# Kernel tuning notes

Hardware: AMD Instinct MI355X
Metric: run time of the kernel (lower is better)

Reference implementation:

```python
import jax, jax.numpy as jnp
import numpy as np

HIDDEN = 768
NUM_HEADS = 12
HEAD_DIM = HIDDEN // NUM_HEADS
B, S = 4, 2048


def setup_inputs() -> dict:
    key = jax.random.key(0)
    ks = jax.random.split(key, 10)
    scale = 1.0 / np.sqrt(HIDDEN)
    return {
        "hidden_states": jax.random.normal(ks[0], (B, S, HIDDEN), dtype=jnp.float32),
        "attention_mask": jnp.ones((B, S), dtype=jnp.float32),
        "Wq": jax.random.normal(ks[1], (HIDDEN, HIDDEN), dtype=jnp.float32) * scale,
        "bq": jnp.zeros((HIDDEN,), dtype=jnp.float32),
        "Wk": jax.random.normal(ks[2], (HIDDEN, HIDDEN), dtype=jnp.float32) * scale,
        "bk": jnp.zeros((HIDDEN,), dtype=jnp.float32),
        "Wv": jax.random.normal(ks[3], (HIDDEN, HIDDEN), dtype=jnp.float32) * scale,
        "bv": jnp.zeros((HIDDEN,), dtype=jnp.float32),
        "Wo": jax.random.normal(ks[4], (HIDDEN, HIDDEN), dtype=jnp.float32) * scale,
        "bo": jnp.zeros((HIDDEN,), dtype=jnp.float32),
    }


def reference(hidden_states, attention_mask, Wq, bq, Wk, bk, Wv, bv, Wo, bo):
    b, s, _ = hidden_states.shape
    # nn.Linear: x @ W.T + b  (W is [out, in])
    Q = hidden_states @ Wq.T + bq
    K = hidden_states @ Wk.T + bk
    V = hidden_states @ Wv.T + bv
    # [b, s, h*d] -> [b, h, s, d]
    Q = Q.reshape(b, s, NUM_HEADS, HEAD_DIM).transpose(0, 2, 1, 3)
    K = K.reshape(b, s, NUM_HEADS, HEAD_DIM).transpose(0, 2, 1, 3)
    V = V.reshape(b, s, NUM_HEADS, HEAD_DIM).transpose(0, 2, 1, 3)
    # scores: [b, h, s, s]
    scores = jnp.einsum("bhqd,bhkd->bhqk", Q, K) / jnp.sqrt(
        jnp.asarray(HEAD_DIM, dtype=Q.dtype))
    # mask: [b, s] -> additive bias broadcast over heads and query dim
    bias = (1.0 - attention_mask)[:, None, None, :] * -10000.0
    scores = scores + bias
    probs = jax.nn.softmax(scores, axis=-1)  # dropout p=0.0 -> identity
    context = jnp.einsum("bhqk,bhkd->bhqd", probs, V)
    context = context.transpose(0, 2, 1, 3).reshape(b, s, HIDDEN)
    return context @ Wo.T + bo
```

## Files before the change

### kernel.cpp

```cpp
#include <hip/hip_runtime.h>
#include <hip/hip_bf16.h>

#define SEQ   2048
#define NH    12
#define MTOK  8192

typedef __attribute__((ext_vector_type(8))) short short8;
typedef __attribute__((ext_vector_type(4))) short short4v;
typedef __attribute__((ext_vector_type(4))) float f32x4;
typedef __attribute__((ext_vector_type(16))) float f32x16;
typedef __attribute__((ext_vector_type(2))) unsigned uint2v;

__device__ inline short f2bf(float x) {
  __hip_bfloat16 h = __float2bfloat16(x);
  return *(short*)&h;
}

#define GLL(gp, lp) __builtin_amdgcn_global_load_lds( \
    (const __attribute__((address_space(1))) void*)(gp), \
    (__attribute__((address_space(3))) void*)(lp), 16, 0, 0)

#define MFMA(a, b, c) __builtin_amdgcn_mfma_f32_16x16x32_bf16(a, b, c, 0, 0, 0)

#if !defined(__HIP_DEVICE_COMPILE__)
#define MFMA32(a, b, c) (c)
#else
#define MFMA32(a, b, c) __builtin_amdgcn_mfma_f32_32x32x16_bf16(a, b, c, 0, 0, 0)
#endif

#if !defined(__HIP_DEVICE_COMPILE__)
#define EXP2(x) (x)
#elif __has_builtin(__builtin_amdgcn_exp2f)
#define EXP2(x) __builtin_amdgcn_exp2f(x)
#else
#define EXP2(x) __expf((x) * 0.6931471805599453f)
#endif

__device__ inline unsigned pack2bf(float a, float b) {
  unsigned ua = __float_as_uint(a) + 0x8000u;
  unsigned ub = __float_as_uint(b) + 0x8000u;
#if defined(__HIP_DEVICE_COMPILE__) && __has_builtin(__builtin_amdgcn_perm)
  return __builtin_amdgcn_perm(ub, ua, 0x07060302u);
#else
  return (ub & 0xFFFF0000u) | (ua >> 16);
#endif
}

__device__ inline unsigned packtrunc2(float a, float b) {
#if defined(__HIP_DEVICE_COMPILE__) && __has_builtin(__builtin_amdgcn_perm)
  return __builtin_amdgcn_perm(__float_as_uint(b), __float_as_uint(a),
                               0x07060302u);
#else
  return (__float_as_uint(b) & 0xFFFF0000u) | (__float_as_uint(a) >> 16);
#endif
}

__device__ inline uint2v lane32swap(unsigned a, unsigned b) {
#if defined(__HIP_DEVICE_COMPILE__) && __has_builtin(__builtin_amdgcn_permlane32_swap)
  return __builtin_amdgcn_permlane32_swap(a, b, false, false);
#else
  int lane = (int)(threadIdx.x & 63);
  unsigned xa = (unsigned)__shfl((int)a, lane ^ 32, 64);
  unsigned xb = (unsigned)__shfl((int)b, lane ^ 32, 64);
  bool hi = lane >= 32;
  uint2v r;
  r.x = hi ? xb : a;
  r.y = hi ? b : xa;
  return r;
#endif
}

union PackFrag {
  unsigned u[2];
  short4v s;
};

union Frag8 {
  unsigned u[4];
  short8 s;
};

#define QSCALE 0.18033688011112042f
#define MBSCALE -14426.950408889634f

__global__ __launch_bounds__(256) void prep(
    const float* __restrict__ hs, const float* __restrict__ Wq,
    const float* __restrict__ Wk, const float* __restrict__ Wv,
    const float* __restrict__ Wo, const float* __restrict__ mask,
    short* __restrict__ Xb, short* __restrict__ Wqkvb,
    short* __restrict__ Wob, float* __restrict__ mbias) {
  int bid = blockIdx.x;
  if (bid < 6144) {
    int i = bid * 256 + threadIdx.x;
    float4 v = ((const float4*)hs)[i];
    short4v o;
    o[0] = f2bf(v.x); o[1] = f2bf(v.y); o[2] = f2bf(v.z); o[3] = f2bf(v.w);
    ((short4v*)Xb)[i] = o;
  } else if (bid < 6144 + 2304) {
    int idx = (bid - 6144) * 256 + threadIdx.x;
    int r = idx / 192, c = (idx - r * 192) * 4;
    const float* src;
    short* dst;
    int rr;
    if (r < 768)       { src = Wq; rr = r;        dst = Wqkvb; }
    else if (r < 1536) { src = Wk; rr = r - 768;  dst = Wqkvb; }
    else if (r < 2304) { src = Wv; rr = r - 1536; dst = Wqkvb; }
    else               { src = Wo; rr = r - 2304; dst = Wob; r = rr; }
    float4 v = *(const float4*)&src[(size_t)rr * 768 + c];
    short4v o;
    o[0] = f2bf(v.x); o[1] = f2bf(v.y); o[2] = f2bf(v.z); o[3] = f2bf(v.w);
    *(short4v*)&dst[(size_t)r * 768 + c] = o;
  } else {
    int i = (bid - 6144 - 2304) * 256 + threadIdx.x;
    if (i < MTOK) mbias[i] = (1.f - mask[i]) * MBSCALE;
  }
}

#define GEMM_BK64_LOOP(Aptr, Bptr)                                            \
  __shared__ __align__(16) short As[128 * 64];                                \
  __shared__ __align__(16) short Bs[128 * 64];                                \
  const int t = threadIdx.x;                                                  \
  const int wid = t >> 6, lane = t & 63, l15 = lane & 15, quad = lane >> 4;   \
  const int bm = blockIdx.x * 128, bn = blockIdx.y * 128;                     \
  const int mq = (wid & 1) * 64, nq = (wid >> 1) * 64;                        \
  const int srow8 = lane >> 3;                                                \
  const int schunk = lane & 7;                                                \
  const int scol = (schunk ^ srow8) * 8;                                      \
  f32x4 acc[4][4] = {};                                                       \
  const short *gA[4], *gB[4];                                                 \
  _Pragma("unroll") for (int g = 0; g < 4; ++g) {                             \
    int row = wid * 32 + g * 8 + srow8;                                       \
    gA[g] = (Aptr) + (size_t)(bm + row) * 768 + scol;                         \
    gB[g] = (Bptr) + (size_t)(bn + row) * 768 + scol;                         \
  }                                                                           \
  for (int k0 = 0; k0 < 768; k0 += 64) {                                      \
    _Pragma("unroll") for (int g = 0; g < 4; ++g)                             \
      GLL(gA[g] + k0, &As[(wid * 32 + g * 8) * 64]);                          \
    _Pragma("unroll") for (int g = 0; g < 4; ++g)                             \
      GLL(gB[g] + k0, &Bs[(wid * 32 + g * 8) * 64]);                          \
    __syncthreads();                                                          \
    _Pragma("unroll") for (int ks = 0; ks < 2; ++ks) {                        \
      short8 a[4], b[4];                                                      \
      _Pragma("unroll") for (int mt = 0; mt < 4; ++mt)                        \
        a[mt] = *(const short8*)&As[(mq + mt * 16 + l15) * 64 +               \
                                    (((ks * 4 + quad) ^ (l15 & 7)) * 8)];     \
      _Pragma("unroll") for (int nt = 0; nt < 4; ++nt)                        \
        b[nt] = *(const short8*)&Bs[(nq + nt * 16 + l15) * 64 +               \
                                    (((ks * 4 + quad) ^ (l15 & 7)) * 8)];     \
      _Pragma("unroll") for (int mt = 0; mt < 4; ++mt)                        \
        _Pragma("unroll") for (int nt = 0; nt < 4; ++nt)                      \
          acc[mt][nt] = MFMA(a[mt], b[nt], acc[mt][nt]);                      \
    }                                                                         \
    __syncthreads();                                                          \
  }

__global__ __launch_bounds__(256) void gemm_qkv(
    const short* __restrict__ A, const short* __restrict__ B,
    const float* __restrict__ bq, const float* __restrict__ bk,
    const float* __restrict__ bv, short* __restrict__ Qb,
    short* __restrict__ Kb, short* __restrict__ Vt) {
  GEMM_BK64_LOOP(A, B)

  const int seg = bn >= 1536 ? 2 : (bn >= 768 ? 1 : 0);
  const float* bias = seg == 0 ? bq : (seg == 1 ? bk : bv);
  const int colbase = bn - seg * 768;

  if (seg < 2) {
    short* dst = seg == 0 ? Qb : Kb;
    const float sc = seg == 0 ? QSCALE : 1.f;
#pragma unroll
    for (int mt = 0; mt < 4; ++mt)
#pragma unroll
      for (int nt = 0; nt < 4; ++nt) {
        int col = colbase + nq + nt * 16 + l15;
        float bias_v = bias[col];
#pragma unroll
        for (int i = 0; i < 4; ++i) {
          int row = bm + mq + mt * 16 + quad * 4 + i;
          dst[(size_t)row * 768 + col] = f2bf((acc[mt][nt][i] + bias_v) * sc);
        }
      }
  } else {
#pragma unroll
    for (int mt = 0; mt < 4; ++mt) {
      int row0 = bm + mq + mt * 16 + quad * 4;
      int b_ = row0 >> 11, s = row0 & 2047;
#pragma unroll
      for (int nt = 0; nt < 4; ++nt) {
        int col = colbase + nq + nt * 16 + l15;
        float bias_v = bias[col];
        int h = col >> 6, d = col & 63;
        short4v pv;
#pragma unroll
        for (int i = 0; i < 4; ++i) pv[i] = f2bf(acc[mt][nt][i] + bias_v);
        *(short4v*)&Vt[(((size_t)b_ * NH + h) * 64 + d) * 2048 + s] = pv;
      }
    }
  }
}

__global__ __launch_bounds__(256) void gemm_out(
    const short* __restrict__ A, const short* __restrict__ B,
    const float* __restrict__ bias, float* __restrict__ C) {
  GEMM_BK64_LOOP(A, B)

#pragma unroll
  for (int mt = 0; mt < 4; ++mt)
#pragma unroll
    for (int nt = 0; nt < 4; ++nt) {
      int col = bn + nq + nt * 16 + l15;
      float bias_v = bias[col];
#pragma unroll
      for (int i = 0; i < 4; ++i) {
        int row = bm + mq + mt * 16 + quad * 4 + i;
        C[(size_t)row * 768 + col] = acc[mt][nt][i] + bias_v;
      }
    }
}

__global__ __launch_bounds__(256, 3) void attn_v12(
    const short* __restrict__ Qb, const short* __restrict__ Kb,
    const short* __restrict__ Vt, const float* __restrict__ maskb,
    short* __restrict__ Ctx) {
  __shared__ __align__(16) short Ks[2][64 * 64];
  __shared__ __align__(16) short Vs[2][64 * 64];
  const int t = threadIdx.x;
  const int w = t >> 6, lane = t & 63, l31 = lane & 31, hi = lane >> 5;
  const int bh = blockIdx.x, b = bh / NH, h = bh % NH;
  const int q0 = blockIdx.y * 128;

  short8 qb[4];
  {
    int rowq = b * 2048 + q0 + w * 32 + l31;
    const short* qp = &Qb[(size_t)rowq * 768 + h * 64 + hi * 8];
#pragma unroll
    for (int kc = 0; kc < 4; ++kc) qb[kc] = *(const short8*)&qp[kc * 16];
  }

  f32x16 O0 = {}, O1 = {}, lacc = {};
  short8 ones8;
#pragma unroll
  for (int j = 0; j < 8; ++j) ones8[j] = (short)0x3F80;

  const int r0 = w * 16 + (lane >> 3);
  const int pc = lane & 7;
  const int swz0 = (pc ^ (r0 & 7)) * 8;
  const int swz1 = (pc ^ ((r0 + 8) & 7)) * 8;
  const short* gK0 = Kb + (size_t)(b * 2048 + r0) * 768 + h * 64 + swz0;
  const short* gK1 = Kb + (size_t)(b * 2048 + r0 + 8) * 768 + h * 64 + swz1;
  const short* gV0 = Vt + ((size_t)bh * 64 + r0) * 2048 + swz0;
  const short* gV1 = Vt + ((size_t)bh * 64 + r0 + 8) * 2048 + swz1;
  const float* mb = maskb + b * 2048;
  const int rs = l31 & 7;

  GLL(gK0, &Ks[0][(w * 16) * 64]);
  GLL(gK1, &Ks[0][(w * 16 + 8) * 64]);
  GLL(gV0, &Vs[0][(w * 16) * 64]);
  GLL(gV1, &Vs[0][(w * 16 + 8) * 64]);

  for (int ti = 0; ti < 32; ++ti) {
    const int cur = ti & 1;
    const int k0 = ti * 64;
    __syncthreads();

    {
      const size_t kn = (size_t)(((ti + 1) & 31) * 64);
      GLL(gK0 + kn * 768, &Ks[1 - cur][(w * 16) * 64]);
      GLL(gK1 + kn * 768, &Ks[1 - cur][(w * 16 + 8) * 64]);
      GLL(gV0 + kn, &Vs[1 - cur][(w * 16) * 64]);
      GLL(gV1 + kn, &Vs[1 - cur][(w * 16 + 8) * 64]);
    }

    short8 pfrag[4];

#pragma unroll
    for (int kb2 = 0; kb2 < 2; ++kb2) {
      f32x16 S;
#pragma unroll
      for (int g = 0; g < 4; ++g) {
        float4 m4 = *(const float4*)&mb[k0 + kb2 * 32 + g * 8 + hi * 4];
        S[4 * g + 0] = m4.x; S[4 * g + 1] = m4.y;
        S[4 * g + 2] = m4.z; S[4 * g + 3] = m4.w;
      }
#pragma unroll
      for (int kc = 0; kc < 4; ++kc) {
        short8 ka = *(const short8*)&Ks[cur][(kb2 * 32 + l31) * 64 +
                                            (((kc * 2 + hi) ^ rs) * 8)];
        S = MFMA32(ka, qb[kc], S);
      }
      unsigned pk[4][2];
#pragma unroll
      for (int g = 0; g < 4; ++g) {
        float p0 = EXP2(S[4 * g + 0]);
        float p1 = EXP2(S[4 * g + 1]);
        float p2 = EXP2(S[4 * g + 2]);
        float p3 = EXP2(S[4 * g + 3]);
        pk[g][0] = packtrunc2(p0, p1);
        pk[g][1] = packtrunc2(p2, p3);
      }
#pragma unroll
      for (int half = 0; half < 2; ++half) {
        Frag8 f;
        uint2v ra = lane32swap(pk[half * 2][0], pk[half * 2 + 1][0]);
        uint2v rb = lane32swap(pk[half * 2][1], pk[half * 2 + 1][1]);
        f.u[0] = ra.x;
        f.u[1] = rb.x;
        f.u[2] = ra.y;
        f.u[3] = rb.y;
        pfrag[kb2 * 2 + half] = f.s;
      }
    }

#pragma unroll
    for (int c = 0; c < 4; ++c) lacc = MFMA32(ones8, pfrag[c], lacc);

#pragma unroll
    for (int c = 0; c < 4; ++c) {
      short8 av0 = *(const short8*)&Vs[cur][(l31) * 64 +
                                           (((c * 2 + hi) ^ rs) * 8)];
      short8 av1 = *(const short8*)&Vs[cur][(32 + l31) * 64 +
                                           (((c * 2 + hi) ^ rs) * 8)];
      O0 = MFMA32(av0, pfrag[c], O0);
      O1 = MFMA32(av1, pfrag[c], O1);
    }
  }

  {
    float inv = 1.f / lacc[0];
    int rowq = b * 2048 + q0 + w * 32 + l31;
    short* cp = &Ctx[(size_t)rowq * 768 + h * 64 + hi * 4];
#pragma unroll
    for (int g = 0; g < 4; ++g) {
      PackFrag pf0, pf1;
      pf0.u[0] = pack2bf(O0[4 * g + 0] * inv, O0[4 * g + 1] * inv);
      pf0.u[1] = pack2bf(O0[4 * g + 2] * inv, O0[4 * g + 3] * inv);
      *(short4v*)&cp[g * 8] = pf0.s;
      pf1.u[0] = pack2bf(O1[4 * g + 0] * inv, O1[4 * g + 1] * inv);
      pf1.u[1] = pack2bf(O1[4 * g + 2] * inv, O1[4 * g + 3] * inv);
      *(short4v*)&cp[32 + g * 8] = pf1.s;
    }
  }
}

extern "C" void kernel_launch(void* const* d_in, const int* in_sizes, int n_in,
                              void* d_out, int out_size, void* d_ws,
                              size_t ws_size, hipStream_t stream) {
  const float* hs   = (const float*)d_in[0];
  const float* mask = (const float*)d_in[1];
  const float* Wq   = (const float*)d_in[2];
  const float* bq   = (const float*)d_in[3];
  const float* Wk   = (const float*)d_in[4];
  const float* bk   = (const float*)d_in[5];
  const float* Wv   = (const float*)d_in[6];
  const float* bv   = (const float*)d_in[7];
  const float* Wo   = (const float*)d_in[8];
  const float* bo   = (const float*)d_in[9];

  char* ws = (char*)d_ws;
  short* Xb    = (short*)(ws);
  short* Wqkvb = (short*)(ws + 12582912);
  short* Wob   = (short*)(ws + 16121856);
  short* Qb    = (short*)(ws + 17301504);
  short* Kb    = (short*)(ws + 29884416);
  short* Vtg   = (short*)(ws + 42467328);
  short* Ctxb  = (short*)(ws + 55050240);
  float* mbias = (float*)(ws + 67633152);

  prep<<<8480, 256, 0, stream>>>(hs, Wq, Wk, Wv, Wo, mask,
                                 Xb, Wqkvb, Wob, mbias);
  gemm_qkv<<<dim3(64, 18), 256, 0, stream>>>(Xb, Wqkvb, bq, bk, bv,
                                             Qb, Kb, Vtg);
  attn_v12<<<dim3(48, 16), 256, 0, stream>>>(Qb, Kb, Vtg, mbias, Ctxb);
  gemm_out<<<dim3(64, 6), 256, 0, stream>>>(Ctxb, Wob, bo, (float*)d_out);
}
```

Baseline: 231.5 us.

## Triple-buffer attention K/V tiles and stage mask bias through LDS

The attention kernel moves from a double-buffered to a triple-buffered K/V LDS pipeline. It issues prefetches two tiles ahead and replaces __syncthreads with a partial vmcnt wait plus a barrier, so more global loads stay in flight. The mask bias is now loaded asynchronously into LDS alongside K/V, instead of being read directly from global memory inside the inner loop. This raises LDS use per block, from 32KB to about 49KB, which may limit occupancy at the declared 3 blocks per CU, and the hand-counted vmcnt has to match the number of loads issued per stage.

```diff
diff --git a/kernel.cpp b/kernel.cpp
--- a/kernel.cpp
+++ b/kernel.cpp
@@ -19,6 +19,10 @@
 #define GLL(gp, lp) __builtin_amdgcn_global_load_lds( \
     (const __attribute__((address_space(1))) void*)(gp), \
     (__attribute__((address_space(3))) void*)(lp), 16, 0, 0)
+
+#define GLL4(gp, lp) __builtin_amdgcn_global_load_lds( \
+    (const __attribute__((address_space(1))) void*)(gp), \
+    (__attribute__((address_space(3))) void*)(lp), 4, 0, 0)
 
 #define MFMA(a, b, c) __builtin_amdgcn_mfma_f32_16x16x32_bf16(a, b, c, 0, 0, 0)
 
@@ -218,12 +222,13 @@
     }
 }
 
-__global__ __launch_bounds__(256, 3) void attn_v12(
+__global__ __launch_bounds__(256, 3) void attn_v13(
     const short* __restrict__ Qb, const short* __restrict__ Kb,
     const short* __restrict__ Vt, const float* __restrict__ maskb,
     short* __restrict__ Ctx) {
-  __shared__ __align__(16) short Ks[2][64 * 64];
-  __shared__ __align__(16) short Vs[2][64 * 64];
+  __shared__ __align__(16) short Ks[3][64 * 64];
+  __shared__ __align__(16) short Vs[3][64 * 64];
+  __shared__ __align__(16) float Mbs[3][64];
   const int t = threadIdx.x;
   const int w = t >> 6, lane = t & 63, l31 = lane & 31, hi = lane >> 5;
   const int bh = blockIdx.x, b = bh / NH, h = bh % NH;
@@ -250,26 +255,32 @@
   const short* gK1 = Kb + (size_t)(b * 2048 + r0 + 8) * 768 + h * 64 + swz1;
   const short* gV0 = Vt + ((size_t)bh * 64 + r0) * 2048 + swz0;
   const short* gV1 = Vt + ((size_t)bh * 64 + r0 + 8) * 2048 + swz1;
-  const float* mb = maskb + b * 2048;
+  const float* gmb = maskb + b * 2048 + lane;
   const int rs = l31 & 7;
 
-  GLL(gK0, &Ks[0][(w * 16) * 64]);
-  GLL(gK1, &Ks[0][(w * 16 + 8) * 64]);
-  GLL(gV0, &Vs[0][(w * 16) * 64]);
-  GLL(gV1, &Vs[0][(w * 16 + 8) * 64]);
-
+#define STAGE(tt, s) do {                                                     \
+    const size_t kn = (size_t)(((tt) & 31) * 64);                             \
+    GLL4(gmb + kn, &Mbs[s][0]);                                               \
+    GLL(gK0 + kn * 768, &Ks[s][(w * 16) * 64]);                               \
+    GLL(gK1 + kn * 768, &Ks[s][(w * 16 + 8) * 64]);                           \
+    GLL(gV0 + kn, &Vs[s][(w * 16) * 64]);                                     \
+    GLL(gV1 + kn, &Vs[s][(w * 16 + 8) * 64]);                                 \
+  } while (0)
+
+#define TILE_SYNC() do {                                                      \
+    asm volatile("s_waitcnt vmcnt(5)" ::: "memory");                          \
+    __builtin_amdgcn_s_barrier();                                             \
+    __builtin_amdgcn_sched_barrier(0);                                        \
+  } while (0)
+
+  STAGE(0, 0);
+  STAGE(1, 1);
+  TILE_SYNC();
+
+  int cur = 0;
   for (int ti = 0; ti < 32; ++ti) {
-    const int cur = ti & 1;
-    const int k0 = ti * 64;
-    __syncthreads();
-
-    {
-      const size_t kn = (size_t)(((ti + 1) & 31) * 64);
-      GLL(gK0 + kn * 768, &Ks[1 - cur][(w * 16) * 64]);
-      GLL(gK1 + kn * 768, &Ks[1 - cur][(w * 16 + 8) * 64]);
-      GLL(gV0 + kn, &Vs[1 - cur][(w * 16) * 64]);
-      GLL(gV1 + kn, &Vs[1 - cur][(w * 16 + 8) * 64]);
-    }
+    const int nx2 = (cur == 0) ? 2 : cur - 1;
+    STAGE(ti + 2, nx2);
 
     short8 pfrag[4];
 
@@ -278,9 +289,9 @@
       f32x16 S;
 #pragma unroll
       for (int g = 0; g < 4; ++g) {
-        float4 m4 = *(const float4*)&mb[k0 + kb2 * 32 + g * 8 + hi * 4];
-        S[4 * g + 0] = m4.x; S[4 * g + 1] = m4.y;
-        S[4 * g + 2] = m4.z; S[4 * g + 3] = m4.w;
+        f32x4 m4 = *(const f32x4*)&Mbs[cur][kb2 * 32 + g * 8 + hi * 4];
+        S[4 * g + 0] = m4[0]; S[4 * g + 1] = m4[1];
+        S[4 * g + 2] = m4[2]; S[4 * g + 3] = m4[3];
       }
 #pragma unroll
       for (int kc = 0; kc < 4; ++kc) {
@@ -323,6 +334,9 @@
       O0 = MFMA32(av0, pfrag[c], O0);
       O1 = MFMA32(av1, pfrag[c], O1);
     }
+
+    TILE_SYNC();
+    cur = (cur == 2) ? 0 : cur + 1;
   }
 
   {
@@ -340,6 +354,8 @@
       *(short4v*)&cp[32 + g * 8] = pf1.s;
     }
   }
+#undef STAGE
+#undef TILE_SYNC
 }
 
 extern "C" void kernel_launch(void* const* d_in, const int* in_sizes, int n_in,
@@ -370,6 +386,6 @@
                                  Xb, Wqkvb, Wob, mbias);
   gemm_qkv<<<dim3(64, 18), 256, 0, stream>>>(Xb, Wqkvb, bq, bk, bv,
                                              Qb, Kb, Vtg);
-  attn_v12<<<dim3(48, 16), 256, 0, stream>>>(Qb, Kb, Vtg, mbias, Ctxb);
+  attn_v13<<<dim3(48, 16), 256, 0, stream>>>(Qb, Kb, Vtg, mbias, Ctxb);
   gemm_out<<<dim3(64, 6), 256, 0, stream>>>(Ctxb, Wob, bo, (float*)d_out);
 }
```

Result: faster. 220.8 us (median of 2 runs) (-4.6%).
